# Performance work log

Measured on AMD Instinct MI355X. Metric: run time of the kernel, lower is better.

The kernel has to match this reference:

```python
import jax, jax.numpy as jnp
import numpy as np

C_DIM = 512
N_TOKEN = 256
N_HEADS = 8
TOKEN_DIM = C_DIM // N_HEADS  # 64


def setup_inputs() -> dict:
    key = jax.random.key(0)
    ks = jax.random.split(key, 8)
    s = 1.0 / np.sqrt(C_DIM)
    W0 = jax.random.normal(ks[0], (4, 8192, C_DIM), dtype=jnp.float32)
    # learnable query tokens (xavier-uniform-ish)
    lim = np.sqrt(6.0 / (N_TOKEN + TOKEN_DIM))
    Q = jax.random.uniform(ks[1], (N_HEADS, N_TOKEN, TOKEN_DIM), minval=-lim, maxval=lim, dtype=jnp.float32)
    kv1_w = jax.random.normal(ks[2], (C_DIM, C_DIM), dtype=jnp.float32) * s
    kv1_b = jnp.zeros((C_DIM,), dtype=jnp.float32)
    qkv2_w = jax.random.normal(ks[3], (TOKEN_DIM, 2 * TOKEN_DIM), dtype=jnp.float32) * (1.0 / np.sqrt(TOKEN_DIM))
    q3_w = jax.random.normal(ks[4], (C_DIM, C_DIM), dtype=jnp.float32) * s
    q3_b = jnp.zeros((C_DIM,), dtype=jnp.float32)
    proj_w = jax.random.normal(ks[5], (C_DIM, C_DIM), dtype=jnp.float32) * s
    proj_b = jnp.zeros((C_DIM,), dtype=jnp.float32)
    return {"W0": W0, "Q": Q, "kv1_w": kv1_w, "kv1_b": kv1_b, "qkv2_w": qkv2_w,
            "q3_w": q3_w, "q3_b": q3_b, "proj_w": proj_w, "proj_b": proj_b}


def reference(W0, Q, kv1_w, kv1_b, qkv2_w, q3_w, q3_b, proj_w, proj_b):
    b, n, c = W0.shape
    h, td = N_HEADS, TOKEN_DIM
    scale = 1.0 / np.sqrt(td)
    # stage 1: compress n nodes into n_token tokens per head
    kv1 = (W0 @ kv1_w + kv1_b).reshape(b, n, h, td).transpose(0, 2, 1, 3)  # b h n c
    pw = jnp.einsum('hmc,bhnc->bhmn', Q, kv1) * scale
    pw = jax.nn.softmax(pw, axis=-1)
    proj_token = jnp.einsum('bhmn,bhnc->bhmc', pw, kv1)  # b h m c
    # stage 2: re-project tokens back to nodes
    kv2 = proj_token @ qkv2_w  # b h m 2c
    k, v = kv2[..., :td], kv2[..., td:]
    q3 = (W0 @ q3_w + q3_b).reshape(b, n, h, td).transpose(0, 2, 1, 3)  # b h n c
    rw = jax.nn.softmax(jnp.einsum('bhnc,bhmc->bhnm', q3, k) * scale, axis=-1)
    W = jnp.einsum('bhnm,bhmc->bhnc', rw, v)
    W = W.transpose(0, 2, 1, 3).reshape(b, n, c)  # b n (h c)
    return W @ proj_w + proj_b
```

## Files before the change

### kernel.cpp

```cpp
#include <hip/hip_runtime.h>
#include <hip/hip_bf16.h>


#define NB 4
#define NSEQ 8192
#define CD 512
#define NH 8
#define TD 64
#define NTOK 256
#define NSPLIT 16
#define NKEYS (NSEQ / NSPLIT)

typedef unsigned short u16;
typedef unsigned int u32;
typedef __bf16 bf16x8 __attribute__((ext_vector_type(8)));
typedef float f32x4 __attribute__((ext_vector_type(4)));
typedef float f32x16 __attribute__((ext_vector_type(16)));

__device__ __forceinline__ u16 f2bf(float f){
  __hip_bfloat16 h = __float2bfloat16(f);
  u16 u; __builtin_memcpy(&u, &h, 2); return u;
}
__device__ __forceinline__ bf16x8 ld8(const u16* p){
  bf16x8 r; __builtin_memcpy(&r, p, 16); return r;
}
__device__ __forceinline__ f32x4 mfma16(bf16x8 a, bf16x8 b, f32x4 c){
  return __builtin_amdgcn_mfma_f32_16x16x32_bf16(a, b, c, 0, 0, 0);
}
__device__ __forceinline__ f32x16 mfma32(bf16x8 a, bf16x8 b, f32x16 c){
  return __builtin_amdgcn_mfma_f32_32x32x16_bf16(a, b, c, 0, 0, 0);
}

__global__ void k_cvt(const float* __restrict__ W0, u16* __restrict__ W0b){
  size_t i = (size_t)blockIdx.x * 256 + threadIdx.x;
  float4 v = ((const float4*)W0)[i];
  u16 w[4] = { f2bf(v.x), f2bf(v.y), f2bf(v.z), f2bf(v.w) };
  __builtin_memcpy(W0b + i*4, w, 8);
}

__global__ void k_prep(const float* __restrict__ kv1_w, const float* __restrict__ q3_w,
                       const float* __restrict__ proj_w, const float* __restrict__ Q,
                       u16* __restrict__ kv1_wt, u16* __restrict__ q3_wt,
                       u16* __restrict__ proj_wt, u16* __restrict__ Qb){
  int i = blockIdx.x * 256 + threadIdx.x;
  int k = i >> 9, n = i & 511;
  kv1_wt [n*CD + k] = f2bf(kv1_w[i]);
  q3_wt  [n*CD + k] = f2bf(q3_w[i] * 0.125f);
  proj_wt[n*CD + k] = f2bf(proj_w[i]);
  if (i < NH*NTOK*TD) Qb[i] = f2bf(Q[i] * 0.125f);
}

__global__ __launch_bounds__(256, 2)
void k_gemm_dual(const u16* __restrict__ A, const u16* __restrict__ B1t,
                 const u16* __restrict__ B2t, const float* __restrict__ bias1,
                 const float* __restrict__ bias2, float bscale2,
                 u16* __restrict__ out1, u16* __restrict__ out2){
  __shared__ __attribute__((aligned(16))) u16 As[128][72];
  __shared__ __attribute__((aligned(16))) u16 B1s[128][72];
  __shared__ __attribute__((aligned(16))) u16 B2s[128][72];
  const int tid = threadIdx.x;
  const int lane = tid & 63, wave = tid >> 6;
  const int l15 = lane & 15, lg = lane >> 4;
  const int wm = (wave >> 1) * 64, wn = (wave & 1) * 64;
  const int bm = blockIdx.x, bn = blockIdx.y;
  f32x4 acc1[4][4] = {}, acc2[4][4] = {};

#pragma unroll 1
  for (int k0 = 0; k0 < CD; k0 += 64){
    __syncthreads();
    {
      int r0 = tid >> 3, c8 = (tid & 7) << 3;
#pragma unroll
      for (int rr = 0; rr < 128; rr += 32){
        const u16* srcA = A   + (size_t)(bm*128 + r0 + rr) * CD + k0 + c8;
        int4 va = *(const int4*)srcA;
        __builtin_memcpy(&As[r0 + rr][c8], &va, 16);
        const u16* s1 = B1t + (size_t)(bn*128 + r0 + rr) * CD + k0 + c8;
        int4 v1 = *(const int4*)s1;
        __builtin_memcpy(&B1s[r0 + rr][c8], &v1, 16);
        const u16* s2 = B2t + (size_t)(bn*128 + r0 + rr) * CD + k0 + c8;
        int4 v2 = *(const int4*)s2;
        __builtin_memcpy(&B2s[r0 + rr][c8], &v2, 16);
      }
    }
    __syncthreads();
#pragma unroll
    for (int ks = 0; ks < 2; ks++){
      bf16x8 af[4], b1f[4], b2f[4];
#pragma unroll
      for (int mf = 0; mf < 4; mf++) af[mf]  = ld8(&As[wm + mf*16 + l15][ks*32 + lg*8]);
#pragma unroll
      for (int nf = 0; nf < 4; nf++){
        b1f[nf] = ld8(&B1s[wn + nf*16 + l15][ks*32 + lg*8]);
        b2f[nf] = ld8(&B2s[wn + nf*16 + l15][ks*32 + lg*8]);
      }
#pragma unroll
      for (int mf = 0; mf < 4; mf++)
#pragma unroll
        for (int nf = 0; nf < 4; nf++){
          acc1[mf][nf] = mfma16(af[mf], b1f[nf], acc1[mf][nf]);
          acc2[mf][nf] = mfma16(af[mf], b2f[nf], acc2[mf][nf]);
        }
    }
  }
#pragma unroll
  for (int nf = 0; nf < 4; nf++){
    int col = bn*128 + wn + nf*16 + l15;
    float bv1 = bias1[col];
    float bv2 = bias2[col] * bscale2;
#pragma unroll
    for (int mf = 0; mf < 4; mf++){
      int row = bm*128 + wm + mf*16 + lg*4;
#pragma unroll
      for (int q = 0; q < 4; q++){
        out1[(size_t)(row + q)*CD + col] = f2bf(acc1[mf][nf][q] + bv1);
        out2[(size_t)(row + q)*CD + col] = f2bf(acc2[mf][nf][q] + bv2);
      }
    }
  }
}

template<int OUT_F32>
__global__ __launch_bounds__(256, 2)
void k_gemm512(const u16* __restrict__ A, const u16* __restrict__ Bt,
               const float* __restrict__ bias, float bscale, void* __restrict__ outp){
  __shared__ __attribute__((aligned(16))) u16 As[128][72];
  __shared__ __attribute__((aligned(16))) u16 Bs[128][72];
  const int tid = threadIdx.x;
  const int lane = tid & 63, wave = tid >> 6;
  const int l15 = lane & 15, lg = lane >> 4;
  const int wm = (wave >> 1) * 64, wn = (wave & 1) * 64;
  const int bm = blockIdx.x, bn = blockIdx.y;
  f32x4 acc[4][4] = {};

#pragma unroll 1
  for (int k0 = 0; k0 < CD; k0 += 64){
    __syncthreads();
    {
      int r0 = tid >> 3, c8 = (tid & 7) << 3;
#pragma unroll
      for (int rr = 0; rr < 128; rr += 32){
        const u16* srcA = A  + (size_t)(bm*128 + r0 + rr) * CD + k0 + c8;
        int4 va = *(const int4*)srcA;
        __builtin_memcpy(&As[r0 + rr][c8], &va, 16);
        const u16* srcB = Bt + (size_t)(bn*128 + r0 + rr) * CD + k0 + c8;
        int4 vb = *(const int4*)srcB;
        __builtin_memcpy(&Bs[r0 + rr][c8], &vb, 16);
      }
    }
    __syncthreads();
#pragma unroll
    for (int ks = 0; ks < 2; ks++){
      bf16x8 af[4], bfr[4];
#pragma unroll
      for (int mf = 0; mf < 4; mf++) af[mf]  = ld8(&As[wm + mf*16 + l15][ks*32 + lg*8]);
#pragma unroll
      for (int nf = 0; nf < 4; nf++) bfr[nf] = ld8(&Bs[wn + nf*16 + l15][ks*32 + lg*8]);
#pragma unroll
      for (int mf = 0; mf < 4; mf++)
#pragma unroll
        for (int nf = 0; nf < 4; nf++)
          acc[mf][nf] = mfma16(af[mf], bfr[nf], acc[mf][nf]);
    }
  }
#pragma unroll
  for (int nf = 0; nf < 4; nf++){
    int col = bn*128 + wn + nf*16 + l15;
    float bv = bias[col] * bscale;
#pragma unroll
    for (int mf = 0; mf < 4; mf++){
      int row = bm*128 + wm + mf*16 + lg*4;
#pragma unroll
      for (int q = 0; q < 4; q++){
        float v = acc[mf][nf][q] + bv;
        if constexpr (OUT_F32) ((float*)outp)[(size_t)(row + q)*CD + col] = v;
        else                   ((u16*)outp)[(size_t)(row + q)*CD + col] = f2bf(v);
      }
    }
  }
}

__global__ __launch_bounds__(256, 3)
void k_attn1(const u16* __restrict__ kv1, const u16* __restrict__ Qb,
             float* __restrict__ o_part, float* __restrict__ ml_part){
  __shared__ __attribute__((aligned(16))) u16 kvs[64][72];
  __shared__ __attribute__((aligned(16))) u16 kvts[64][72];
  const int tid = threadIdx.x, lane = tid & 63, wave = tid >> 6;
  const int bh = blockIdx.x, mt = blockIdx.y, s = blockIdx.z;
  const int b = bh >> 3, h = bh & 7;
  const int l31 = lane & 31, hi = lane >> 5;
  const int m0 = mt*128 + wave*32;

  bf16x8 bq[4];
#pragma unroll
  for (int ks = 0; ks < 4; ks++)
    bq[ks] = ld8(Qb + (size_t)(h*NTOK + m0 + l31)*TD + ks*16 + hi*8);

  float mrun = -1e30f, srun = 0.f;
  f32x16 o0 = {}, o1 = {};

#pragma unroll 1
  for (int c = 0; c < NKEYS/64; c++){
    const int nc = s*NKEYS + c*64;
    __syncthreads();
    {
      int r = tid >> 2, sg = tid & 3, seg = sg * 16;
      const u16* src = kv1 + (size_t)(b*NSEQ + nc + r)*CD + h*TD + seg;
      int4 v0 = *(const int4*)src;
      int4 v1 = *(const int4*)(src + 8);
      __builtin_memcpy(&kvs[r][seg],     &v0, 16);
      __builtin_memcpy(&kvs[r][seg + 8], &v1, 16);
      u16 tmp[16];
      __builtin_memcpy(tmp,     &v0, 16);
      __builtin_memcpy(tmp + 8, &v1, 16);
#pragma unroll
      for (int j = 0; j < 16; j++){
        int jj = (j + 2*sg) & 15;
        kvts[seg + jj][r] = tmp[jj];
      }
    }
    __syncthreads();
#pragma unroll
    for (int sub = 0; sub < 2; sub++){
      f32x16 t = {};
#pragma unroll
      for (int ks = 0; ks < 4; ks++){
        bf16x8 ak = ld8(&kvs[sub*32 + l31][ks*16 + hi*8]);
        t = mfma32(ak, bq[ks], t);
      }
      float c0 = fmaxf(fmaxf(t[0], t[1]),  fmaxf(t[2], t[3]));
      float c1 = fmaxf(fmaxf(t[4], t[5]),  fmaxf(t[6], t[7]));
      float c2 = fmaxf(fmaxf(t[8], t[9]),  fmaxf(t[10], t[11]));
      float c3 = fmaxf(fmaxf(t[12], t[13]), fmaxf(t[14], t[15]));
      float cm = fmaxf(fmaxf(c0, c1), fmaxf(c2, c3));
      cm = fmaxf(cm, __shfl_xor(cm, 32, 64));
      if (!__all(cm <= mrun + 8.f)){
        float mnew = fmaxf(mrun, cm);
        float corr = __expf(mrun - mnew);
        srun *= corr;
#pragma unroll
        for (int r = 0; r < 16; r++){ o0[r] *= corr; o1[r] *= corr; }
        mrun = mnew;
      }
      u32 w[8], x[8];
      float ls = 0.f;
#pragma unroll
      for (int j = 0; j < 8; j++){
        float e0 = __expf(t[2*j]     - mrun);
        float e1 = __expf(t[2*j + 1] - mrun);
        ls += e0 + e1;
        w[j] = (u32)f2bf(e0) | ((u32)f2bf(e1) << 16);
      }
      srun += ls;
#pragma unroll
      for (int j = 0; j < 8; j++) x[j] = __shfl_xor(w[j], 32, 64);
#pragma unroll
      for (int c2i = 0; c2i < 2; c2i++){
        u32 arr[4];
        arr[0] = hi ? x[4*c2i + 2] : w[4*c2i + 0];
        arr[1] = hi ? x[4*c2i + 3] : w[4*c2i + 1];
        arr[2] = hi ? w[4*c2i + 2] : x[4*c2i + 0];
        arr[3] = hi ? w[4*c2i + 3] : x[4*c2i + 1];
        bf16x8 pb; __builtin_memcpy(&pb, arr, 16);
        bf16x8 av0 = ld8(&kvts[l31][sub*32 + c2i*16 + hi*8]);
        bf16x8 av1 = ld8(&kvts[l31 + 32][sub*32 + c2i*16 + hi*8]);
        o0 = mfma32(av0, pb, o0);
        o1 = mfma32(av1, pb, o1);
      }
    }
  }
  float rs = srun + __shfl_xor(srun, 32, 64);

  const size_t pbase = (size_t)(bh*NSPLIT + s);
  float* qrow = o_part + (pbase*NTOK + m0 + l31)*TD;
#pragma unroll
  for (int g = 0; g < 4; g++){
    float4 v0 = make_float4(o0[4*g+0], o0[4*g+1], o0[4*g+2], o0[4*g+3]);
    *(float4*)(qrow + 8*g + 4*hi) = v0;
    float4 v1 = make_float4(o1[4*g+0], o1[4*g+1], o1[4*g+2], o1[4*g+3]);
    *(float4*)(qrow + 32 + 8*g + 4*hi) = v1;
  }
  if (hi == 0){
    ml_part[(pbase*2)*NTOK + m0 + l31]     = mrun;
    ml_part[(pbase*2 + 1)*NTOK + m0 + l31] = rs;
  }
}

__global__ __launch_bounds__(256, 2)
void k_comb(const float* __restrict__ o_part, const float* __restrict__ ml_part,
            const float* __restrict__ qkv2_w, u16* __restrict__ kb, u16* __restrict__ vtb){
  __shared__ float w2[TD*2*TD];
  __shared__ float osh[16][68];
  const int tid = threadIdx.x;
  const int bh = blockIdx.x >> 4, mtile = blockIdx.x & 15;
  const int m0 = mtile * 16;
  for (int i = tid; i < TD*2*TD/4; i += 256) ((float4*)w2)[i] = ((const float4*)qkv2_w)[i];

  const int mi = tid >> 4, tj = tid & 15;
  const int m = m0 + mi;
  float M = -1e30f;
#pragma unroll
  for (int s = 0; s < NSPLIT; s++)
    M = fmaxf(M, ml_part[(size_t)((bh*NSPLIT + s)*2)*NTOK + m]);
  float4 acc = make_float4(0.f,0.f,0.f,0.f);
  float denom = 0.f;
#pragma unroll 1
  for (int s = 0; s < NSPLIT; s++){
    size_t base = (size_t)(bh*NSPLIT + s);
    float w = __expf(ml_part[(base*2)*NTOK + m] - M);
    denom += ml_part[(base*2 + 1)*NTOK + m] * w;
    float4 v = ((const float4*)(o_part + (base*NTOK + m)*TD))[tj];
    acc.x += w*v.x; acc.y += w*v.y; acc.z += w*v.z; acc.w += w*v.w;
  }
  float inv = 1.f / denom;
  osh[mi][tj*4+0] = acc.x*inv; osh[mi][tj*4+1] = acc.y*inv;
  osh[mi][tj*4+2] = acc.z*inv; osh[mi][tj*4+3] = acc.w*inv;
  __syncthreads();
  const int j0 = tj * 8;
  float o8[8] = {};
#pragma unroll
  for (int t = 0; t < TD; t++){
    float ov = osh[mi][t];
#pragma unroll
    for (int jj = 0; jj < 8; jj++) o8[jj] += ov * w2[t*2*TD + j0 + jj];
  }
  if (j0 < TD){
#pragma unroll
    for (int jj = 0; jj < 8; jj++)
      kb[(size_t)(bh*NTOK + m)*TD + j0 + jj] = f2bf(o8[jj]);
  } else {
#pragma unroll
    for (int jj = 0; jj < 8; jj++)
      vtb[(size_t)(bh*TD + (j0 - TD + jj))*NTOK + m] = f2bf(o8[jj]);
  }
}

__global__ __launch_bounds__(256, 2)
void k_attn2(const u16* __restrict__ q3, const u16* __restrict__ kb,
             const u16* __restrict__ vtb, u16* __restrict__ Wout){
  __shared__ __attribute__((aligned(16))) u16 buf[32768];
  u16* kbs = buf;
  u16* vts = buf + 16384;
  const int tid = threadIdx.x, lane = tid & 63, wave = tid >> 6;
  const int bh = blockIdx.x >> 6, nt = blockIdx.x & 63;
  const int b = bh >> 3, h = bh & 7;
  const int l31 = lane & 31, hi = lane >> 5;
  const int n0 = nt * 128 + wave * 32;

  bf16x8 bq[4];
#pragma unroll
  for (int ks = 0; ks < 4; ks++)
    bq[ks] = ld8(q3 + (size_t)(b*NSEQ + n0 + l31)*CD + h*TD + ks*16 + hi*8);

  {
    const u16* ksrc = kb + (size_t)bh*NTOK*TD;
#pragma unroll
    for (int it = 0; it < 8; it++){
      int idx = it*256 + tid;
      int r = idx >> 3, g = idx & 7;
      int4 v; __builtin_memcpy(&v, ksrc + r*64 + g*8, 16);
      __builtin_memcpy(kbs + r*64 + ((g ^ (r & 7)) << 3), &v, 16);
    }
    const u16* vsrc = vtb + (size_t)bh*TD*NTOK;
#pragma unroll
    for (int it = 0; it < 8; it++){
      int idx = it*256 + tid;
      int t = idx >> 5, g = idx & 31;
      int4 v; __builtin_memcpy(&v, vsrc + t*256 + g*8, 16);
      __builtin_memcpy(vts + t*256 + ((g ^ (t & 31)) << 3), &v, 16);
    }
  }
  __syncthreads();

  f32x16 p[8] = {};
  __builtin_amdgcn_s_setprio(1);
#pragma unroll
  for (int kt = 0; kt < 8; kt++){
#pragma unroll
    for (int ks = 0; ks < 4; ks++){
      int r = kt*32 + l31, g = ks*2 + hi;
      bf16x8 ak = ld8(kbs + r*64 + ((g ^ (r & 7)) << 3));
      p[kt] = mfma32(ak, bq[ks], p[kt]);
    }
  }
  __builtin_amdgcn_s_setprio(0);

  float mx0 = -1e30f, mx1 = -1e30f, mx2 = -1e30f, mx3 = -1e30f;
#pragma unroll
  for (int kt = 0; kt < 8; kt++){
#pragma unroll
    for (int r = 0; r < 16; r += 4){
      mx0 = fmaxf(mx0, p[kt][r+0]); mx1 = fmaxf(mx1, p[kt][r+1]);
      mx2 = fmaxf(mx2, p[kt][r+2]); mx3 = fmaxf(mx3, p[kt][r+3]);
    }
  }
  float m = fmaxf(fmaxf(mx0, mx1), fmaxf(mx2, mx3));
  m = fmaxf(m, __shfl_xor(m, 32, 64));
  float s0 = 0.f, s1 = 0.f, s2 = 0.f, s3 = 0.f;
#pragma unroll
  for (int kt = 0; kt < 8; kt++){
#pragma unroll
    for (int r = 0; r < 16; r += 4){
      float e0 = __expf(p[kt][r+0] - m); p[kt][r+0] = e0; s0 += e0;
      float e1 = __expf(p[kt][r+1] - m); p[kt][r+1] = e1; s1 += e1;
      float e2 = __expf(p[kt][r+2] - m); p[kt][r+2] = e2; s2 += e2;
      float e3 = __expf(p[kt][r+3] - m); p[kt][r+3] = e3; s3 += e3;
    }
  }
  float rs = (s0 + s1) + (s2 + s3);
  rs += __shfl_xor(rs, 32, 64);
  const float inv = 1.f / rs;

  f32x16 o0 = {}, o1 = {};
#pragma unroll
  for (int kt = 0; kt < 8; kt++){
    u32 w[8], x[8];
#pragma unroll
    for (int j = 0; j < 8; j++){
      u32 lo = f2bf(p[kt][2*j]);
      u32 hh = f2bf(p[kt][2*j + 1]);
      w[j] = lo | (hh << 16);
    }
#pragma unroll
    for (int j = 0; j < 8; j++) x[j] = __shfl_xor(w[j], 32, 64);
    __builtin_amdgcn_s_setprio(1);
#pragma unroll
    for (int c = 0; c < 2; c++){
      u32 arr[4];
      arr[0] = hi ? x[4*c + 2] : w[4*c + 0];
      arr[1] = hi ? x[4*c + 3] : w[4*c + 1];
      arr[2] = hi ? w[4*c + 2] : x[4*c + 0];
      arr[3] = hi ? w[4*c + 3] : x[4*c + 1];
      bf16x8 pb; __builtin_memcpy(&pb, arr, 16);
      int g = kt*4 + c*2 + hi;
      bf16x8 av0 = ld8(vts + l31*256        + ((g ^ l31) << 3));
      bf16x8 av1 = ld8(vts + (l31+32)*256   + ((g ^ l31) << 3));
      o0 = mfma32(av0, pb, o0);
      o1 = mfma32(av1, pb, o1);
    }
    __builtin_amdgcn_s_setprio(0);
  }

  __syncthreads();
  u16 (*osh)[32][68] = (u16 (*)[32][68])buf;
#pragma unroll
  for (int r = 0; r < 16; r++){
    int row = (r & 3) + 8*(r >> 2) + 4*hi;
    osh[wave][l31][row]      = f2bf(o0[r] * inv);
    osh[wave][l31][32 + row] = f2bf(o1[r] * inv);
  }
  const u16* src = &osh[wave][l31][hi*32];
  int4 v0, v1, v2, v3;
  __builtin_memcpy(&v0, src,      16);
  __builtin_memcpy(&v1, src + 8,  16);
  __builtin_memcpy(&v2, src + 16, 16);
  __builtin_memcpy(&v3, src + 24, 16);
  u16* dst = Wout + (size_t)(b*NSEQ + n0 + l31)*CD + h*TD + hi*32;
  __builtin_memcpy(dst,      &v0, 16);
  __builtin_memcpy(dst + 8,  &v1, 16);
  __builtin_memcpy(dst + 16, &v2, 16);
  __builtin_memcpy(dst + 24, &v3, 16);
}

extern "C" void kernel_launch(void* const* d_in, const int* in_sizes, int n_in,
                              void* d_out, int out_size, void* d_ws, size_t ws_size,
                              hipStream_t stream){
  const float* W0     = (const float*)d_in[0];
  const float* Q      = (const float*)d_in[1];
  const float* kv1_w  = (const float*)d_in[2];
  const float* kv1_b  = (const float*)d_in[3];
  const float* qkv2_w = (const float*)d_in[4];
  const float* q3_w   = (const float*)d_in[5];
  const float* q3_b   = (const float*)d_in[6];
  const float* proj_w = (const float*)d_in[7];
  const float* proj_b = (const float*)d_in[8];
  (void)in_sizes; (void)n_in; (void)out_size; (void)ws_size;

  char* ws = (char*)d_ws;
  u16*   W0b     = (u16*)  (ws);
  u16*   kv1_ws  = (u16*)  (ws + ((size_t)32<<20));
  float* o_part  = (float*)(ws + ((size_t)64<<20));
  float* ml_part = (float*)(ws + ((size_t)96<<20));
  u16*   kv1_wt  = (u16*)  (ws + ((size_t)97<<20));
  u16*   q3_wt   = (u16*)  (ws + ((size_t)97<<20) + (1<<19));
  u16*   proj_wt = (u16*)  (ws + ((size_t)98<<20));
  u16*   Qb      = (u16*)  (ws + ((size_t)98<<20) + (1<<19));
  u16*   kb      = (u16*)  (ws + ((size_t)99<<20));
  u16*   vtb     = (u16*)  (ws + ((size_t)100<<20));
  u16*   W_ws    = (u16*)  (ws + ((size_t)32<<20));
  u16*   q3s     = (u16*)  d_out;

  k_cvt<<<16384, 256, 0, stream>>>(W0, W0b);
  k_prep<<<1024, 256, 0, stream>>>(kv1_w, q3_w, proj_w, Q, kv1_wt, q3_wt, proj_wt, Qb);
  k_gemm_dual<<<dim3(256,4), 256, 0, stream>>>(W0b, kv1_wt, q3_wt, kv1_b, q3_b, 0.125f,
                                               kv1_ws, q3s);
  k_attn1<<<dim3(NB*NH, 2, NSPLIT), 256, 0, stream>>>(kv1_ws, Qb, o_part, ml_part);
  k_comb<<<NB*NH*16, 256, 0, stream>>>(o_part, ml_part, qkv2_w, kb, vtb);
  k_attn2<<<NB*NH*64, 256, 0, stream>>>(q3s, kb, vtb, W_ws);
  k_gemm512<1><<<dim3(256,4), 256, 0, stream>>>(W_ws, proj_wt, proj_b, 1.0f, (void*)d_out);
}
```

Measured before the change: 213.6 us.

## Split dual-output GEMM into two single GEMMs and pack transpose stores

Replaces the fused dual GEMM, which computed both the kv1 and q3 projections from one A tile, with two launches of a single-output GEMM that keeps half the accumulators and raises the launch-bounds occupancy target to 3 blocks per CU. It gives up the reuse of the W0 A-tile across both outputs, so W0b is read twice, in exchange for lower register and LDS pressure. The attention-1 LDS transpose now loads 32-bit words and rotates them with lane-dependent selects instead of indexing a 16-element u16 array by a lane-dependent offset, aiming to avoid scratch-memory spills.

```diff
diff --git a/kernel.cpp b/kernel.cpp
--- a/kernel.cpp
+++ b/kernel.cpp
@@ -50,20 +50,17 @@
   if (i < NH*NTOK*TD) Qb[i] = f2bf(Q[i] * 0.125f);
 }
 
-__global__ __launch_bounds__(256, 2)
-void k_gemm_dual(const u16* __restrict__ A, const u16* __restrict__ B1t,
-                 const u16* __restrict__ B2t, const float* __restrict__ bias1,
-                 const float* __restrict__ bias2, float bscale2,
-                 u16* __restrict__ out1, u16* __restrict__ out2){
+__global__ __launch_bounds__(256, 3)
+void k_gemm512_b16(const u16* __restrict__ A, const u16* __restrict__ Bt,
+                   const float* __restrict__ bias, float bscale, u16* __restrict__ outp){
   __shared__ __attribute__((aligned(16))) u16 As[128][72];
-  __shared__ __attribute__((aligned(16))) u16 B1s[128][72];
-  __shared__ __attribute__((aligned(16))) u16 B2s[128][72];
+  __shared__ __attribute__((aligned(16))) u16 Bs[128][72];
   const int tid = threadIdx.x;
   const int lane = tid & 63, wave = tid >> 6;
   const int l15 = lane & 15, lg = lane >> 4;
   const int wm = (wave >> 1) * 64, wn = (wave & 1) * 64;
   const int bm = blockIdx.x, bn = blockIdx.y;
-  f32x4 acc1[4][4] = {}, acc2[4][4] = {};
+  f32x4 acc[4][4] = {};
 
 #pragma unroll 1
   for (int k0 = 0; k0 < CD; k0 += 64){
@@ -72,50 +69,39 @@
       int r0 = tid >> 3, c8 = (tid & 7) << 3;
 #pragma unroll
       for (int rr = 0; rr < 128; rr += 32){
-        const u16* srcA = A   + (size_t)(bm*128 + r0 + rr) * CD + k0 + c8;
+        const u16* srcA = A  + (size_t)(bm*128 + r0 + rr) * CD + k0 + c8;
         int4 va = *(const int4*)srcA;
         __builtin_memcpy(&As[r0 + rr][c8], &va, 16);
-        const u16* s1 = B1t + (size_t)(bn*128 + r0 + rr) * CD + k0 + c8;
-        int4 v1 = *(const int4*)s1;
-        __builtin_memcpy(&B1s[r0 + rr][c8], &v1, 16);
-        const u16* s2 = B2t + (size_t)(bn*128 + r0 + rr) * CD + k0 + c8;
-        int4 v2 = *(const int4*)s2;
-        __builtin_memcpy(&B2s[r0 + rr][c8], &v2, 16);
+        const u16* srcB = Bt + (size_t)(bn*128 + r0 + rr) * CD + k0 + c8;
+        int4 vb = *(const int4*)srcB;
+        __builtin_memcpy(&Bs[r0 + rr][c8], &vb, 16);
       }
     }
     __syncthreads();
 #pragma unroll
     for (int ks = 0; ks < 2; ks++){
-      bf16x8 af[4], b1f[4], b2f[4];
+      bf16x8 af[4], bfr[4];
 #pragma unroll
       for (int mf = 0; mf < 4; mf++) af[mf]  = ld8(&As[wm + mf*16 + l15][ks*32 + lg*8]);
 #pragma unroll
-      for (int nf = 0; nf < 4; nf++){
-        b1f[nf] = ld8(&B1s[wn + nf*16 + l15][ks*32 + lg*8]);
-        b2f[nf] = ld8(&B2s[wn + nf*16 + l15][ks*32 + lg*8]);
-      }
+      for (int nf = 0; nf < 4; nf++) bfr[nf] = ld8(&Bs[wn + nf*16 + l15][ks*32 + lg*8]);
 #pragma unroll
       for (int mf = 0; mf < 4; mf++)
 #pragma unroll
-        for (int nf = 0; nf < 4; nf++){
-          acc1[mf][nf] = mfma16(af[mf], b1f[nf], acc1[mf][nf]);
-          acc2[mf][nf] = mfma16(af[mf], b2f[nf], acc2[mf][nf]);
-        }
+        for (int nf = 0; nf < 4; nf++)
+          acc[mf][nf] = mfma16(af[mf], bfr[nf], acc[mf][nf]);
     }
   }
 #pragma unroll
   for (int nf = 0; nf < 4; nf++){
     int col = bn*128 + wn + nf*16 + l15;
-    float bv1 = bias1[col];
-    float bv2 = bias2[col] * bscale2;
+    float bv = bias[col] * bscale;
 #pragma unroll
     for (int mf = 0; mf < 4; mf++){
       int row = bm*128 + wm + mf*16 + lg*4;
 #pragma unroll
-      for (int q = 0; q < 4; q++){
-        out1[(size_t)(row + q)*CD + col] = f2bf(acc1[mf][nf][q] + bv1);
-        out2[(size_t)(row + q)*CD + col] = f2bf(acc2[mf][nf][q] + bv2);
-      }
+      for (int q = 0; q < 4; q++)
+        outp[(size_t)(row + q)*CD + col] = f2bf(acc[mf][nf][q] + bv);
     }
   }
 }
@@ -210,13 +196,19 @@
       int4 v1 = *(const int4*)(src + 8);
       __builtin_memcpy(&kvs[r][seg],     &v0, 16);
       __builtin_memcpy(&kvs[r][seg + 8], &v1, 16);
-      u16 tmp[16];
-      __builtin_memcpy(tmp,     &v0, 16);
-      __builtin_memcpy(tmp + 8, &v1, 16);
-#pragma unroll
-      for (int j = 0; j < 16; j++){
-        int jj = (j + 2*sg) & 15;
-        kvts[seg + jj][r] = tmp[jj];
+      u32 tr[8];
+      __builtin_memcpy(tr,     &v0, 16);
+      __builtin_memcpy(tr + 4, &v1, 16);
+      u32 t1[8], t2[8];
+#pragma unroll
+      for (int i = 0; i < 8; i++) t1[i] = (sg & 1) ? tr[(i + 1) & 7] : tr[i];
+#pragma unroll
+      for (int i = 0; i < 8; i++) t2[i] = (sg & 2) ? t1[(i + 2) & 7] : t1[i];
+#pragma unroll
+      for (int j2 = 0; j2 < 8; j2++){
+        int jj = (2*j2 + 2*sg) & 15;
+        kvts[seg + jj][r]     = (u16)(t2[j2] & 0xffff);
+        kvts[seg + jj + 1][r] = (u16)(t2[j2] >> 16);
       }
     }
     __syncthreads();
@@ -492,8 +484,8 @@
 
   k_cvt<<<16384, 256, 0, stream>>>(W0, W0b);
   k_prep<<<1024, 256, 0, stream>>>(kv1_w, q3_w, proj_w, Q, kv1_wt, q3_wt, proj_wt, Qb);
-  k_gemm_dual<<<dim3(256,4), 256, 0, stream>>>(W0b, kv1_wt, q3_wt, kv1_b, q3_b, 0.125f,
-                                               kv1_ws, q3s);
+  k_gemm512_b16<<<dim3(256,4), 256, 0, stream>>>(W0b, kv1_wt, kv1_b, 1.0f, kv1_ws);
+  k_gemm512_b16<<<dim3(256,4), 256, 0, stream>>>(W0b, q3_wt, q3_b, 0.125f, q3s);
   k_attn1<<<dim3(NB*NH, 2, NSPLIT), 256, 0, stream>>>(kv1_ws, Qb, o_part, ml_part);
   k_comb<<<NB*NH*16, 256, 0, stream>>>(o_part, ml_part, qkv2_w, kb, vtb);
   k_attn2<<<NB*NH*64, 256, 0, stream>>>(q3s, kb, vtb, W_ws);
```

Result: no change. 216.8 us (+1.5%).
